# Optimization experiments

Hardware: AMD Instinct MI355X
Metric: run time of the kernel (lower is better)

## Reference

```python
import jax, jax.numpy as jnp
import numpy as np

D = 128
N_COLS = 64
EPS = 1e-6
# op MLP index per feature token: mult, add, cos, absdiff, sub_ab, sub_ba, div_ab, div_ba
MLP_IDX = np.array([0, 1, 2, 3, 4, 4, 5, 5])


def setup_inputs() -> dict:
    key = jax.random.key(0)
    ks = jax.random.split(key, 16)
    B = 64
    pairs = np.array([(i, j) for i in range(N_COLS) for j in range(i + 1, N_COLS)], dtype=np.int32)
    P = pairs.shape[0]  # 2016
    s = 0.02
    inp = {
        "x": jax.random.normal(ks[0], (B, N_COLS, D), dtype=jnp.float32),
        "presence": jax.random.randint(ks[1], (B, N_COLS), 0, 2, dtype=jnp.int32),
        "idx_i": jnp.asarray(pairs[:, 0]),
        "idx_j": jnp.asarray(pairs[:, 1]),
        # 6 op MLPs (multiply, add, cosine, abs_diff, subtract, divide): d -> d/2 -> d
        "ops_W1": jax.random.normal(ks[2], (6, D, D // 2), dtype=jnp.float32) * s,
        "ops_b1": jnp.zeros((6, D // 2), dtype=jnp.float32),
        "ops_W2": jax.random.normal(ks[3], (6, D // 2, D), dtype=jnp.float32) * s,
        "ops_b2": jnp.zeros((6, D), dtype=jnp.float32),
        # presence MLP: 4 -> d/2 -> d
        "pres_W1": jax.random.normal(ks[4], (4, D // 2), dtype=jnp.float32) * s,
        "pres_b1": jnp.zeros((D // 2,), dtype=jnp.float32),
        "pres_W2": jax.random.normal(ks[5], (D // 2, D), dtype=jnp.float32) * s,
        "pres_b2": jnp.zeros((D,), dtype=jnp.float32),
        # fusion MLP: 9d -> 2d -> d
        "fus_W1": jax.random.normal(ks[6], (9 * D, 2 * D), dtype=jnp.float32) * s,
        "fus_b1": jnp.zeros((2 * D,), dtype=jnp.float32),
        "fus_W2": jax.random.normal(ks[7], (2 * D, D), dtype=jnp.float32) * s,
        "fus_b2": jnp.zeros((D,), dtype=jnp.float32),
    }
    return inp


def reference(x, presence, idx_i, idx_j,
              ops_W1, ops_b1, ops_W2, ops_b2,
              pres_W1, pres_b1, pres_W2, pres_b2,
              fus_W1, fus_b1, fus_W2, fus_b2):
    B = x.shape[0]
    P = idx_i.shape[0]
    A = x[:, idx_i]  # [B, P, D]
    Bv = x[:, idx_j]  # [B, P, D]
    An = A / (jnp.linalg.norm(A, axis=-1, keepdims=True) + EPS)
    Bn = Bv / (jnp.linalg.norm(Bv, axis=-1, keepdims=True) + EPS)
    # 8 elementwise relation features [8, B, P, D]
    feats = jnp.stack([
        A * Bv,                 # multiply
        A + Bv,                 # add
        An * Bn,                # cosine (elementwise normalized product)
        jnp.abs(A - Bv),        # abs diff
        A - Bv,                 # subtract A->B
        Bv - A,                 # subtract B->A
        A / (Bv + EPS),         # divide A/B
        Bv / (A + EPS),         # divide B/A
    ])
    W1 = ops_W1[MLP_IDX]  # [8, D, D/2]
    b1 = ops_b1[MLP_IDX]
    W2 = ops_W2[MLP_IDX]
    b2 = ops_b2[MLP_IDX]
    h = jax.nn.relu(jnp.einsum('kbpd,kdh->kbph', feats, W1) + b1[:, None, None, :])
    tok = jnp.einsum('kbph,khd->kbpd', h, W2) + b2[:, None, None, :]  # [8, B, P, D]
    # presence flags [B, P, 4]
    pa = presence[:, idx_i].astype(x.dtype)
    pb = presence[:, idx_j].astype(x.dtype)
    flags = jnp.stack([pa * pb, pa * (1 - pb), (1 - pa) * pb, (1 - pa) * (1 - pb)], axis=-1)
    ptok = jax.nn.relu(flags @ pres_W1 + pres_b1) @ pres_W2 + pres_b2  # [B, P, D]
    # concat 9 tokens -> fusion MLP -> 1 token per pair
    cat = jnp.concatenate([jnp.transpose(tok, (1, 2, 0, 3)).reshape(B, P, 8 * D), ptok], axis=-1)
    out = jax.nn.relu(cat @ fus_W1 + fus_b1) @ fus_W2 + fus_b2  # [B, P, D]
    return out
```

## Files before the change

### kernel.cpp

```cpp
#include <hip/hip_runtime.h>

#define EPS 1e-6f

using bfrag = __attribute__((ext_vector_type(8))) short;
using ffrag = __attribute__((ext_vector_type(4))) float;
typedef unsigned short ushortT;

#define MFMA(a, b, c) __builtin_amdgcn_mfma_f32_16x16x32_bf16((a), (b), (c), 0, 0, 0)

__device__ __forceinline__ ushortT bf_hi(float x) {
  unsigned u = __builtin_bit_cast(unsigned, x);
  return (ushortT)((u + 0x7FFFu + ((u >> 16) & 1u)) >> 16);
}
__device__ __forceinline__ float uaf(unsigned u) { return __builtin_bit_cast(float, u); }
__device__ __forceinline__ unsigned cvtpk(float a, float b) {
  unsigned d;
  asm("v_cvt_pk_bf16_f32 %0, %1, %2" : "=v"(d) : "v"(a), "v"(b));
  return d;
}
__device__ __forceinline__ int op_of(int k) { return (k < 4) ? k : ((k >> 1) + 2); }

__global__ void prologue(const float* __restrict__ ops_W1,
                         const float* __restrict__ ops_W2,
                         const float* __restrict__ ops_b2,
                         const float* __restrict__ pres_W1,
                         const float* __restrict__ pres_b1,
                         const float* __restrict__ pres_W2,
                         const float* __restrict__ pres_b2,
                         const float* __restrict__ fus_W1,
                         const float* __restrict__ fus_b1,
                         const float* __restrict__ fus_W2,
                         ushortT* __restrict__ Gp,
                         ushortT* __restrict__ W1p,
                         ushortT* __restrict__ W2p,
                         float* __restrict__ cb) {
  const int blk = blockIdx.x;
  const int tid = threadIdx.x;

  if (blk < 512) {
    int r = blk, n = tid;
    int slot = r >> 6;
    const int KMAP[8] = {0, 2, 3, 4, 1, 5, 6, 7};
    int k = KMAP[slot];
    int op = op_of(k);
    const float* w2 = ops_W2 + (size_t)(op * 64 + (r & 63)) * 128;
    const float* w1 = fus_W1 + (size_t)(k * 128) * 256 + n;
    float a0 = 0.f, a1 = 0.f, a2 = 0.f, a3 = 0.f;
#pragma unroll 8
    for (int d = 0; d < 128; d += 4) {
      a0 = fmaf(w2[d], w1[(size_t)d * 256], a0);
      a1 = fmaf(w2[d + 1], w1[(size_t)(d + 1) * 256], a1);
      a2 = fmaf(w2[d + 2], w1[(size_t)(d + 2) * 256], a2);
      a3 = fmaf(w2[d + 3], w1[(size_t)(d + 3) * 256], a3);
    }
    float acc = (a0 + a1) + (a2 + a3);
    int nt = n >> 4, kk = r >> 5, quad = (r >> 3) & 3, j = r & 7;
    int lane = quad * 16 + (n & 15);
    Gp[((nt * 16 + kk) * 64 + lane) * 8 + j] = bf_hi(acc);
  } else if (blk < 544) {
    int gid = (blk - 512) * 256 + tid;
    int lane = gid & 63, kk = (gid >> 6) & 3, nt = (gid >> 8) & 3, k = gid >> 10;
    int op = op_of(k);
    int col = nt * 16 + (lane & 15);
#pragma unroll
    for (int j = 0; j < 8; ++j) {
      int d = kk * 32 + ((lane >> 4) & 3) * 8 + j;
      W1p[gid * 8 + j] = bf_hi(ops_W1[((size_t)op * 128 + d) * 64 + col]);
    }
  } else if (blk < 560) {
    int gid = (blk - 544) * 256 + tid;
    int lane = gid & 63, kk = (gid >> 6) & 7, nt = gid >> 9;
    int col = nt * 16 + (lane & 15);
#pragma unroll
    for (int j = 0; j < 8; ++j) {
      int d = kk * 32 + ((lane >> 4) & 3) * 8 + j;
      W2p[gid * 8 + j] = bf_hi(fus_W2[(size_t)d * 128 + col]);
    }
  } else {
    int c = blk - 560, n = tid;
    __shared__ float hrelu[64];
    __shared__ float ptok[128];
    if (n < 64) hrelu[n] = fmaxf(pres_W1[c * 64 + n] + pres_b1[n], 0.f);
    __syncthreads();
    if (n < 128) {
      float p0 = pres_b2[n], p1 = 0.f;
#pragma unroll 8
      for (int hh = 0; hh < 64; hh += 2) {
        p0 = fmaf(hrelu[hh], pres_W2[hh * 128 + n], p0);
        p1 = fmaf(hrelu[hh + 1], pres_W2[(hh + 1) * 128 + n], p1);
      }
      ptok[n] = p0 + p1;
    }
    __syncthreads();
    float acc = fus_b1[n];
#pragma unroll 4
    for (int d = 0; d < 128; ++d)
      acc = fmaf(ptok[d], fus_W1[(size_t)(1024 + d) * 256 + n], acc);
    float acc2 = 0.f;
    for (int k = 0; k < 8; ++k) {
      int op = op_of(k);
#pragma unroll 4
      for (int d = 0; d < 128; ++d)
        acc2 = fmaf(ops_b2[op * 128 + d], fus_W1[(size_t)(k * 128 + d) * 256 + n], acc2);
    }
    cb[c * 256 + n] = acc + acc2;
  }
}

__device__ __forceinline__ void ldX(const float* Xrow, int quad, float (&r)[32]) {
#pragma unroll
  for (int kk = 0; kk < 4; ++kk) {
    float4 t0 = *(const float4*)(Xrow + kk * 32 + quad * 8);
    float4 t1 = *(const float4*)(Xrow + kk * 32 + quad * 8 + 4);
    r[kk * 8 + 0] = t0.x; r[kk * 8 + 1] = t0.y; r[kk * 8 + 2] = t0.z; r[kk * 8 + 3] = t0.w;
    r[kk * 8 + 4] = t1.x; r[kk * 8 + 5] = t1.y; r[kk * 8 + 6] = t1.z; r[kk * 8 + 7] = t1.w;
  }
}

struct Frag2 {
  bfrag h[4];
  bfrag l[4];
};

union U4 {
  unsigned u[4];
  bfrag b;
};

#define FM_MUL 0
#define FM_ADD 1
#define FM_SUB 2
#define FM_ABS 3
#define FM_DAB 4
#define FM_DBA 5

template <int M>
__device__ __forceinline__ void buildFrags(const float (&af)[32], const float (&bf)[32],
                                           Frag2& fr) {
#pragma unroll
  for (int kk = 0; kk < 4; ++kk) {
    U4 uh, ul;
#pragma unroll
    for (int p = 0; p < 4; ++p) {
      float a0 = af[kk * 8 + 2 * p],     b0 = bf[kk * 8 + 2 * p];
      float a1 = af[kk * 8 + 2 * p + 1], b1 = bf[kk * 8 + 2 * p + 1];
      float f0, f1;
      if constexpr (M == FM_MUL)      { f0 = a0 * b0; f1 = a1 * b1; }
      else if constexpr (M == FM_ADD) { f0 = a0 + b0; f1 = a1 + b1; }
      else if constexpr (M == FM_SUB) { f0 = a0 - b0; f1 = a1 - b1; }
      else if constexpr (M == FM_ABS) { f0 = fabsf(a0 - b0); f1 = fabsf(a1 - b1); }
      else if constexpr (M == FM_DAB) {
        f0 = a0 * __builtin_amdgcn_rcpf(b0 + EPS);
        f1 = a1 * __builtin_amdgcn_rcpf(b1 + EPS);
      } else {
        f0 = b0 * __builtin_amdgcn_rcpf(a0 + EPS);
        f1 = b1 * __builtin_amdgcn_rcpf(a1 + EPS);
      }
      unsigned dh = cvtpk(f0, f1);
      float r0 = f0 - uaf(dh << 16);
      float r1 = f1 - uaf(dh & 0xFFFF0000u);
      uh.u[p] = dh;
      ul.u[p] = cvtpk(r0, r1);
    }
    fr.h[kk] = uh.b;
    fr.l[kk] = ul.b;
  }
}

template <int K>
__device__ __forceinline__ void mmAll(const Frag2& fr, int lane,
                                      const ushortT* __restrict__ W1p, ffrag (&s)[4]) {
#pragma unroll
  for (int nt = 0; nt < 4; ++nt) {
    const ushortT* wp = W1p + ((K * 4 + nt) * 4) * 512 + lane * 8;
    ffrag acc = {0.f, 0.f, 0.f, 0.f};
#pragma unroll
    for (int kk = 0; kk < 4; ++kk) {
      bfrag w = *(const bfrag*)(wp + kk * 512);
      acc = MFMA(fr.h[kk], w, acc);
      acc = MFMA(fr.l[kk], w, acc);
    }
    s[nt] = acc;
  }
}

__device__ __forceinline__ void ldBias(const float* __restrict__ ops_b1, int OP, int c0,
                                       float (&bb)[4]) {
#pragma unroll
  for (int nt = 0; nt < 4; ++nt) bb[nt] = ops_b1[OP * 64 + nt * 16 + c0];
}

__device__ __forceinline__ void storeH(ffrag s, float scl, float bias, int rbase, int col,
                                       ushortT (*Hh)[136], ushortT (*Hl)[136]) {
  float v[4];
#pragma unroll
  for (int i = 0; i < 4; ++i) v[i] = fmaxf(fmaf(s[i], scl, bias), 0.f);
#pragma unroll
  for (int p = 0; p < 2; ++p) {
    unsigned dh = cvtpk(v[2 * p], v[2 * p + 1]);
    float r0 = v[2 * p] - uaf(dh << 16);
    float r1 = v[2 * p + 1] - uaf(dh & 0xFFFF0000u);
    unsigned dl = cvtpk(r0, r1);
    Hh[rbase + 2 * p][col] = (ushortT)(dh & 0xFFFFu);
    Hh[rbase + 2 * p + 1][col] = (ushortT)(dh >> 16);
    Hl[rbase + 2 * p][col] = (ushortT)(dl & 0xFFFFu);
    Hl[rbase + 2 * p + 1][col] = (ushortT)(dl >> 16);
  }
}

__device__ __forceinline__ void storeH4(const ffrag (&s)[4], float scl, const float (&bb)[4],
                                        int rbase, int colbase, int c0,
                                        ushortT (*Hh)[136], ushortT (*Hl)[136]) {
#pragma unroll
  for (int nt = 0; nt < 4; ++nt)
    storeH(s[nt], scl, bb[nt], rbase, colbase + nt * 16 + c0, Hh, Hl);
}

__device__ __forceinline__ void p3round(int r, int wv, int lane, int quad, int c0,
                                        ushortT (*Hh)[136], ushortT (*Hl)[136],
                                        const ushortT* __restrict__ Gp,
                                        ffrag (&u)[4], ffrag (&v)[4]) {
#pragma unroll
  for (int kk = 0; kk < 4; ++kk) {
    bfrag ah0 = *(const bfrag*)&Hh[c0][kk * 32 + quad * 8];
    bfrag al0 = *(const bfrag*)&Hl[c0][kk * 32 + quad * 8];
    bfrag ah1 = *(const bfrag*)&Hh[16 + c0][kk * 32 + quad * 8];
    bfrag al1 = *(const bfrag*)&Hl[16 + c0][kk * 32 + quad * 8];
#pragma unroll
    for (int nt4 = 0; nt4 < 4; ++nt4) {
      bfrag g = *(const bfrag*)(Gp + (((wv * 4 + nt4) * 16 + r * 4 + kk) * 64 + lane) * 8);
      u[nt4] = MFMA(ah0, g, u[nt4]);
      u[nt4] = MFMA(al0, g, u[nt4]);
      v[nt4] = MFMA(ah1, g, v[nt4]);
      v[nt4] = MFMA(al1, g, v[nt4]);
    }
  }
}

__global__ __launch_bounds__(256, 3)
void drel_main(const float* __restrict__ x, const int* __restrict__ presence,
               const int* __restrict__ idx_i, const int* __restrict__ idx_j,
               const float* __restrict__ ops_b1, const float* __restrict__ fus_b2,
               const ushortT* __restrict__ W1p, const ushortT* __restrict__ Gp,
               const ushortT* __restrict__ W2p, const float* __restrict__ cbias,
               float* __restrict__ out) {
  __shared__ __align__(16) char smem[51328];
  float   (*Xs)[132]  = reinterpret_cast<float(*)[132]>(smem);
  ushortT (*Hh)[136]  = reinterpret_cast<ushortT(*)[136]>(smem + 33792);
  ushortT (*Hl)[136]  = reinterpret_cast<ushortT(*)[136]>(smem + 42496);
  ushortT (*Dh)[264]  = reinterpret_cast<ushortT(*)[264]>(smem + 33792);
  int* sCombo = reinterpret_cast<int*>(smem + 51200);

  const int tid = threadIdx.x;
  const int wv = tid >> 6, lane = tid & 63, quad = lane >> 4, c0 = lane & 15;
  const int wtile = wv & 1;
  const int wrole = wv >> 1;

  const int blk = blockIdx.x;
  const int b = blk / 63;
  const int p0 = (blk % 63) * 32;

  const float* xb = x + (size_t)b * 64 * 128;
#pragma unroll
  for (int it = 0; it < 8; ++it) {
    int i = tid + it * 256;
    int row = i >> 5, c4 = (i & 31) * 4;
    *(float4*)&Xs[row][c4] = *(const float4*)(xb + row * 128 + c4);
  }
  if (tid < 32) {
    int p = p0 + tid;
    int pa = presence[b * 64 + idx_i[p]];
    int pb = presence[b * 64 + idx_j[p]];
    sCombo[tid] = pa ? (pb ? 0 : 1) : (pb ? 2 : 3);
  }

  const int rI = idx_i[p0 + wtile * 16 + c0];
  const int rJ = idx_j[p0 + wtile * 16 + c0];
  const int rbase = wtile * 16 + quad * 4;

  ffrag u[4], v[4];
  __syncthreads();
  {
    int comb0[4], comb1[4];
#pragma unroll
    for (int i = 0; i < 4; ++i) {
      comb0[i] = sCombo[quad * 4 + i];
      comb1[i] = sCombo[16 + quad * 4 + i];
    }
#pragma unroll
    for (int nt4 = 0; nt4 < 4; ++nt4) {
      int col = (wv * 4 + nt4) * 16 + c0;
#pragma unroll
      for (int i = 0; i < 4; ++i) {
        u[nt4][i] = cbias[comb0[i] * 256 + col];
        v[nt4][i] = cbias[comb1[i] * 256 + col];
      }
    }
  }

  float af[32], bf[32];
  Frag2 fr;
  ffrag s4[4];

  {
    ldX(Xs[rI], quad, af); ldX(Xs[rJ], quad, bf);
    buildFrags<FM_MUL>(af, bf, fr);
    ffrag s[4];
    float bb[4];
    if (wrole == 0) {
      ldBias(ops_b1, 0, c0, bb);
      mmAll<0>(fr, lane, W1p, s);
      storeH4(s, 1.f, bb, rbase, 0, c0, Hh, Hl);
    } else {
      float sa = 0.f, sb = 0.f;
#pragma unroll
      for (int q = 0; q < 32; ++q) { sa = fmaf(af[q], af[q], sa); sb = fmaf(bf[q], bf[q], sb); }
      sa += __shfl_xor(sa, 16); sb += __shfl_xor(sb, 16);
      sa += __shfl_xor(sa, 32); sb += __shfl_xor(sb, 32);
      float scl = (1.f / (sqrtf(sa) + EPS)) * (1.f / (sqrtf(sb) + EPS));
      ldBias(ops_b1, 2, c0, bb);
      mmAll<2>(fr, lane, W1p, s);
      storeH4(s, scl, bb, rbase, 64, c0, Hh, Hl);
    }
  }
  __syncthreads();
  p3round(0, wv, lane, quad, c0, Hh, Hl, Gp, u, v);
  __syncthreads();

  {
    ldX(Xs[rI], quad, af); ldX(Xs[rJ], quad, bf);
    float bb[4];
    if (wrole == 0) {
      buildFrags<FM_ABS>(af, bf, fr);
      ffrag s[4];
      ldBias(ops_b1, 3, c0, bb);
      mmAll<3>(fr, lane, W1p, s);
      storeH4(s, 1.f, bb, rbase, 0, c0, Hh, Hl);
    } else {
      buildFrags<FM_SUB>(af, bf, fr);
      ldBias(ops_b1, 4, c0, bb);
      mmAll<4>(fr, lane, W1p, s4);
      storeH4(s4, 1.f, bb, rbase, 64, c0, Hh, Hl);
    }
  }
  __syncthreads();
  p3round(1, wv, lane, quad, c0, Hh, Hl, Gp, u, v);
  __syncthreads();

  {
    float bb[4];
    if (wrole == 0) {
      ldX(Xs[rI], quad, af); ldX(Xs[rJ], quad, bf);
      buildFrags<FM_ADD>(af, bf, fr);
      ffrag s[4];
      ldBias(ops_b1, 1, c0, bb);
      mmAll<1>(fr, lane, W1p, s);
      storeH4(s, 1.f, bb, rbase, 0, c0, Hh, Hl);
    } else {
      ldBias(ops_b1, 4, c0, bb);
      storeH4(s4, -1.f, bb, rbase, 64, c0, Hh, Hl);
    }
  }
  __syncthreads();
  p3round(2, wv, lane, quad, c0, Hh, Hl, Gp, u, v);
  __syncthreads();

  {
    ldX(Xs[rI], quad, af); ldX(Xs[rJ], quad, bf);
    ffrag s[4];
    float bb[4];
    ldBias(ops_b1, 5, c0, bb);
    if (wrole == 0) {
      buildFrags<FM_DAB>(af, bf, fr);
      mmAll<6>(fr, lane, W1p, s);
      storeH4(s, 1.f, bb, rbase, 0, c0, Hh, Hl);
    } else {
      buildFrags<FM_DBA>(af, bf, fr);
      mmAll<7>(fr, lane, W1p, s);
      storeH4(s, 1.f, bb, rbase, 64, c0, Hh, Hl);
    }
  }
  __syncthreads();
  p3round(3, wv, lane, quad, c0, Hh, Hl, Gp, u, v);
  __syncthreads();

#pragma unroll
  for (int nt4 = 0; nt4 < 4; ++nt4) {
    int col = (wv * 4 + nt4) * 16 + c0;
#pragma unroll
    for (int p = 0; p < 2; ++p) {
      unsigned du = cvtpk(fmaxf(u[nt4][2 * p], 0.f), fmaxf(u[nt4][2 * p + 1], 0.f));
      Dh[quad * 4 + 2 * p][col] = (ushortT)(du & 0xFFFFu);
      Dh[quad * 4 + 2 * p + 1][col] = (ushortT)(du >> 16);
      unsigned dv = cvtpk(fmaxf(v[nt4][2 * p], 0.f), fmaxf(v[nt4][2 * p + 1], 0.f));
      Dh[16 + quad * 4 + 2 * p][col] = (ushortT)(dv & 0xFFFFu);
      Dh[16 + quad * 4 + 2 * p + 1][col] = (ushortT)(dv >> 16);
    }
  }
  __syncthreads();

  ffrag o[2], q[2];
#pragma unroll
  for (int nt2 = 0; nt2 < 2; ++nt2) {
    float bias = fus_b2[(wv * 2 + nt2) * 16 + c0];
    o[nt2] = ffrag{bias, bias, bias, bias};
    q[nt2] = o[nt2];
  }
#pragma unroll
  for (int kk = 0; kk < 8; ++kk) {
    bfrag dh0 = *(const bfrag*)&Dh[c0][kk * 32 + quad * 8];
    bfrag dh1 = *(const bfrag*)&Dh[16 + c0][kk * 32 + quad * 8];
#pragma unroll
    for (int nt2 = 0; nt2 < 2; ++nt2) {
      bfrag w = *(const bfrag*)(W2p + (((wv * 2 + nt2) * 8 + kk) * 64 + lane) * 8);
      o[nt2] = MFMA(dh0, w, o[nt2]);
      q[nt2] = MFMA(dh1, w, q[nt2]);
    }
  }
#pragma unroll
  for (int nt2 = 0; nt2 < 2; ++nt2) {
    int col = (wv * 2 + nt2) * 16 + c0;
#pragma unroll
    for (int i = 0; i < 4; ++i) {
      int row = quad * 4 + i;
      out[(size_t)(b * 2016 + p0 + row) * 128 + col] = o[nt2][i];
      out[(size_t)(b * 2016 + p0 + 16 + row) * 128 + col] = q[nt2][i];
    }
  }
}

extern "C" void kernel_launch(void* const* d_in, const int* in_sizes, int n_in,
                              void* d_out, int out_size, void* d_ws, size_t ws_size,
                              hipStream_t stream) {
  const float* x        = (const float*)d_in[0];
  const int*   presence = (const int*)d_in[1];
  const int*   idx_i    = (const int*)d_in[2];
  const int*   idx_j    = (const int*)d_in[3];
  const float* ops_W1   = (const float*)d_in[4];
  const float* ops_b1   = (const float*)d_in[5];
  const float* ops_W2   = (const float*)d_in[6];
  const float* ops_b2   = (const float*)d_in[7];
  const float* pres_W1  = (const float*)d_in[8];
  const float* pres_b1  = (const float*)d_in[9];
  const float* pres_W2  = (const float*)d_in[10];
  const float* pres_b2  = (const float*)d_in[11];
  const float* fus_W1   = (const float*)d_in[12];
  const float* fus_b1   = (const float*)d_in[13];
  const float* fus_W2   = (const float*)d_in[14];
  const float* fus_b2   = (const float*)d_in[15];

  char* ws = (char*)d_ws;
  ushortT* Gp  = (ushortT*)(ws);
  ushortT* W1p = (ushortT*)(ws + 262144);
  ushortT* W2p = (ushortT*)(ws + 393216);
  float*   CB  = (float*)(ws + 458752);

  prologue<<<564, 256, 0, stream>>>(ops_W1, ops_W2, ops_b2, pres_W1, pres_b1,
                                    pres_W2, pres_b2, fus_W1, fus_b1, fus_W2,
                                    Gp, W1p, W2p, CB);
  drel_main<<<4032, 256, 0, stream>>>(x, presence, idx_i, idx_j, ops_b1, fus_b2,
                                      W1p, Gp, W2p, CB, (float*)d_out);
}
```

Measured before the change: 259.8 us.

## Use single-pass fp16 MFMA for bounded ops instead of split bf16 hi/lo

For the six well-bounded feature ops (mul, add, cos, abs, sub), the kernel now packs the features, the op W1 weights and the fused W2·fusW1 product into fp16 and does one fp16 MFMA per step. Before, it split each value into bf16 high and low parts and ran two bf16 MFMAs. The division ops keep the split-bf16 path because their values can be very large. This halves MFMA count and LDS traffic for most rounds. In exchange it takes on fp16 range and precision risk on the activations and weights.

```diff
diff --git a/kernel.cpp b/kernel.cpp
--- a/kernel.cpp
+++ b/kernel.cpp
@@ -3,10 +3,12 @@
 #define EPS 1e-6f
 
 using bfrag = __attribute__((ext_vector_type(8))) short;
+using hfrag = __attribute__((ext_vector_type(8))) _Float16;
 using ffrag = __attribute__((ext_vector_type(4))) float;
 typedef unsigned short ushortT;
 
 #define MFMA(a, b, c) __builtin_amdgcn_mfma_f32_16x16x32_bf16((a), (b), (c), 0, 0, 0)
+#define MFMA16(a, b, c) __builtin_amdgcn_mfma_f32_16x16x32_f16((a), (b), (c), 0, 0, 0)
 
 __device__ __forceinline__ ushortT bf_hi(float x) {
   unsigned u = __builtin_bit_cast(unsigned, x);
@@ -16,6 +18,11 @@
 __device__ __forceinline__ unsigned cvtpk(float a, float b) {
   unsigned d;
   asm("v_cvt_pk_bf16_f32 %0, %1, %2" : "=v"(d) : "v"(a), "v"(b));
+  return d;
+}
+__device__ __forceinline__ unsigned pkf16(float a, float b) {
+  unsigned d;
+  asm("v_cvt_pkrtz_f16_f32 %0, %1, %2" : "=v"(d) : "v"(a), "v"(b));
   return d;
 }
 __device__ __forceinline__ int op_of(int k) { return (k < 4) ? k : ((k >> 1) + 2); }
@@ -54,9 +61,16 @@
       a3 = fmaf(w2[d + 3], w1[(size_t)(d + 3) * 256], a3);
     }
     float acc = (a0 + a1) + (a2 + a3);
+    ushortT outv;
+    if (slot < 6) {
+      _Float16 hv = (_Float16)acc;
+      outv = __builtin_bit_cast(ushortT, hv);
+    } else {
+      outv = bf_hi(acc);
+    }
     int nt = n >> 4, kk = r >> 5, quad = (r >> 3) & 3, j = r & 7;
     int lane = quad * 16 + (n & 15);
-    Gp[((nt * 16 + kk) * 64 + lane) * 8 + j] = bf_hi(acc);
+    Gp[((nt * 16 + kk) * 64 + lane) * 8 + j] = outv;
   } else if (blk < 544) {
     int gid = (blk - 512) * 256 + tid;
     int lane = gid & 63, kk = (gid >> 6) & 3, nt = (gid >> 8) & 3, k = gid >> 10;
@@ -65,7 +79,15 @@
 #pragma unroll
     for (int j = 0; j < 8; ++j) {
       int d = kk * 32 + ((lane >> 4) & 3) * 8 + j;
-      W1p[gid * 8 + j] = bf_hi(ops_W1[((size_t)op * 128 + d) * 64 + col]);
+      float w = ops_W1[((size_t)op * 128 + d) * 64 + col];
+      ushortT outv;
+      if (k < 6) {
+        _Float16 hv = (_Float16)w;
+        outv = __builtin_bit_cast(ushortT, hv);
+      } else {
+        outv = bf_hi(w);
+      }
+      W1p[gid * 8 + j] = outv;
     }
   } else if (blk < 560) {
     int gid = (blk - 544) * 256 + tid;
@@ -135,11 +157,11 @@
 #define FM_DBA 5
 
 template <int M>
-__device__ __forceinline__ void buildFrags(const float (&af)[32], const float (&bf)[32],
-                                           Frag2& fr) {
+__device__ __forceinline__ void buildFragsF16(const float (&af)[32], const float (&bf)[32],
+                                              bfrag (&h)[4]) {
 #pragma unroll
   for (int kk = 0; kk < 4; ++kk) {
-    U4 uh, ul;
+    U4 uh;
 #pragma unroll
     for (int p = 0; p < 4; ++p) {
       float a0 = af[kk * 8 + 2 * p],     b0 = bf[kk * 8 + 2 * p];
@@ -148,8 +170,25 @@
       if constexpr (M == FM_MUL)      { f0 = a0 * b0; f1 = a1 * b1; }
       else if constexpr (M == FM_ADD) { f0 = a0 + b0; f1 = a1 + b1; }
       else if constexpr (M == FM_SUB) { f0 = a0 - b0; f1 = a1 - b1; }
-      else if constexpr (M == FM_ABS) { f0 = fabsf(a0 - b0); f1 = fabsf(a1 - b1); }
-      else if constexpr (M == FM_DAB) {
+      else                            { f0 = fabsf(a0 - b0); f1 = fabsf(a1 - b1); }
+      uh.u[p] = pkf16(f0, f1);
+    }
+    h[kk] = uh.b;
+  }
+}
+
+template <int M>
+__device__ __forceinline__ void buildFrags(const float (&af)[32], const float (&bf)[32],
+                                           Frag2& fr) {
+#pragma unroll
+  for (int kk = 0; kk < 4; ++kk) {
+    U4 uh, ul;
+#pragma unroll
+    for (int p = 0; p < 4; ++p) {
+      float a0 = af[kk * 8 + 2 * p],     b0 = bf[kk * 8 + 2 * p];
+      float a1 = af[kk * 8 + 2 * p + 1], b1 = bf[kk * 8 + 2 * p + 1];
+      float f0, f1;
+      if constexpr (M == FM_DAB) {
         f0 = a0 * __builtin_amdgcn_rcpf(b0 + EPS);
         f1 = a1 * __builtin_amdgcn_rcpf(b1 + EPS);
       } else {
@@ -168,6 +207,22 @@
 }
 
 template <int K>
+__device__ __forceinline__ void mmAllF16(const bfrag (&h)[4], int lane,
+                                         const ushortT* __restrict__ W1p, ffrag (&s)[4]) {
+#pragma unroll
+  for (int nt = 0; nt < 4; ++nt) {
+    const ushortT* wp = W1p + ((K * 4 + nt) * 4) * 512 + lane * 8;
+    ffrag acc = {0.f, 0.f, 0.f, 0.f};
+#pragma unroll
+    for (int kk = 0; kk < 4; ++kk) {
+      hfrag w = __builtin_bit_cast(hfrag, *(const bfrag*)(wp + kk * 512));
+      acc = MFMA16(__builtin_bit_cast(hfrag, h[kk]), w, acc);
+    }
+    s[nt] = acc;
+  }
+}
+
+template <int K>
 __device__ __forceinline__ void mmAll(const Frag2& fr, int lane,
                                       const ushortT* __restrict__ W1p, ffrag (&s)[4]) {
 #pragma unroll
@@ -190,11 +245,32 @@
   for (int nt = 0; nt < 4; ++nt) bb[nt] = ops_b1[OP * 64 + nt * 16 + c0];
 }
 
-__device__ __forceinline__ void storeH(ffrag s, float scl, float bias, int rbase, int col,
+__device__ __forceinline__ void storeHf(ffrag s, float scl, float bias, int rbase, int col,
+                                        ushortT (*Hh)[136]) {
+  float v[4];
+#pragma unroll
+  for (int i = 0; i < 4; ++i) v[i] = fmaxf(fmaf(s[i], scl, bias), 0.f);
+#pragma unroll
+  for (int p = 0; p < 2; ++p) {
+    unsigned d = pkf16(v[2 * p], v[2 * p + 1]);
+    Hh[rbase + 2 * p][col] = (ushortT)(d & 0xFFFFu);
+    Hh[rbase + 2 * p + 1][col] = (ushortT)(d >> 16);
+  }
+}
+
+__device__ __forceinline__ void storeHf4(const ffrag (&s)[4], float scl, const float (&bb)[4],
+                                         int rbase, int colbase, int c0,
+                                         ushortT (*Hh)[136]) {
+#pragma unroll
+  for (int nt = 0; nt < 4; ++nt)
+    storeHf(s[nt], scl, bb[nt], rbase, colbase + nt * 16 + c0, Hh);
+}
+
+__device__ __forceinline__ void storeH(ffrag s, float bias, int rbase, int col,
                                        ushortT (*Hh)[136], ushortT (*Hl)[136]) {
   float v[4];
 #pragma unroll
-  for (int i = 0; i < 4; ++i) v[i] = fmaxf(fmaf(s[i], scl, bias), 0.f);
+  for (int i = 0; i < 4; ++i) v[i] = fmaxf(s[i] + bias, 0.f);
 #pragma unroll
   for (int p = 0; p < 2; ++p) {
     unsigned dh = cvtpk(v[2 * p], v[2 * p + 1]);
@@ -208,12 +284,30 @@
   }
 }
 
-__device__ __forceinline__ void storeH4(const ffrag (&s)[4], float scl, const float (&bb)[4],
+__device__ __forceinline__ void storeH4(const ffrag (&s)[4], const float (&bb)[4],
                                         int rbase, int colbase, int c0,
                                         ushortT (*Hh)[136], ushortT (*Hl)[136]) {
 #pragma unroll
   for (int nt = 0; nt < 4; ++nt)
-    storeH(s[nt], scl, bb[nt], rbase, colbase + nt * 16 + c0, Hh, Hl);
+    storeH(s[nt], bb[nt], rbase, colbase + nt * 16 + c0, Hh, Hl);
+}
+
+__device__ __forceinline__ void p3roundF16(int r, int wv, int lane, int quad, int c0,
+                                           ushortT (*Hh)[136],
+                                           const ushortT* __restrict__ Gp,
+                                           ffrag (&u)[4], ffrag (&v)[4]) {
+#pragma unroll
+  for (int kk = 0; kk < 4; ++kk) {
+    hfrag ah0 = __builtin_bit_cast(hfrag, *(const bfrag*)&Hh[c0][kk * 32 + quad * 8]);
+    hfrag ah1 = __builtin_bit_cast(hfrag, *(const bfrag*)&Hh[16 + c0][kk * 32 + quad * 8]);
+#pragma unroll
+    for (int nt4 = 0; nt4 < 4; ++nt4) {
+      hfrag g = __builtin_bit_cast(
+          hfrag, *(const bfrag*)(Gp + (((wv * 4 + nt4) * 16 + r * 4 + kk) * 64 + lane) * 8));
+      u[nt4] = MFMA16(ah0, g, u[nt4]);
+      v[nt4] = MFMA16(ah1, g, v[nt4]);
+    }
+  }
 }
 
 __device__ __forceinline__ void p3round(int r, int wv, int lane, int quad, int c0,
@@ -299,18 +393,18 @@
   }
 
   float af[32], bf[32];
-  Frag2 fr;
+  bfrag fh[4];
   ffrag s4[4];
 
   {
     ldX(Xs[rI], quad, af); ldX(Xs[rJ], quad, bf);
-    buildFrags<FM_MUL>(af, bf, fr);
+    buildFragsF16<FM_MUL>(af, bf, fh);
     ffrag s[4];
     float bb[4];
     if (wrole == 0) {
       ldBias(ops_b1, 0, c0, bb);
-      mmAll<0>(fr, lane, W1p, s);
-      storeH4(s, 1.f, bb, rbase, 0, c0, Hh, Hl);
+      mmAllF16<0>(fh, lane, W1p, s);
+      storeHf4(s, 1.f, bb, rbase, 0, c0, Hh);
     } else {
       float sa = 0.f, sb = 0.f;
 #pragma unroll
@@ -319,65 +413,66 @@
       sa += __shfl_xor(sa, 32); sb += __shfl_xor(sb, 32);
       float scl = (1.f / (sqrtf(sa) + EPS)) * (1.f / (sqrtf(sb) + EPS));
       ldBias(ops_b1, 2, c0, bb);
-      mmAll<2>(fr, lane, W1p, s);
-      storeH4(s, scl, bb, rbase, 64, c0, Hh, Hl);
-    }
-  }
-  __syncthreads();
-  p3round(0, wv, lane, quad, c0, Hh, Hl, Gp, u, v);
+      mmAllF16<2>(fh, lane, W1p, s);
+      storeHf4(s, scl, bb, rbase, 64, c0, Hh);
+    }
+  }
+  __syncthreads();
+  p3roundF16(0, wv, lane, quad, c0, Hh, Gp, u, v);
   __syncthreads();
 
   {
     ldX(Xs[rI], quad, af); ldX(Xs[rJ], quad, bf);
     float bb[4];
     if (wrole == 0) {
-      buildFrags<FM_ABS>(af, bf, fr);
+      buildFragsF16<FM_ABS>(af, bf, fh);
       ffrag s[4];
       ldBias(ops_b1, 3, c0, bb);
-      mmAll<3>(fr, lane, W1p, s);
-      storeH4(s, 1.f, bb, rbase, 0, c0, Hh, Hl);
+      mmAllF16<3>(fh, lane, W1p, s);
+      storeHf4(s, 1.f, bb, rbase, 0, c0, Hh);
     } else {
-      buildFrags<FM_SUB>(af, bf, fr);
+      buildFragsF16<FM_SUB>(af, bf, fh);
       ldBias(ops_b1, 4, c0, bb);
-      mmAll<4>(fr, lane, W1p, s4);
-      storeH4(s4, 1.f, bb, rbase, 64, c0, Hh, Hl);
-    }
-  }
-  __syncthreads();
-  p3round(1, wv, lane, quad, c0, Hh, Hl, Gp, u, v);
+      mmAllF16<4>(fh, lane, W1p, s4);
+      storeHf4(s4, 1.f, bb, rbase, 64, c0, Hh);
+    }
+  }
+  __syncthreads();
+  p3roundF16(1, wv, lane, quad, c0, Hh, Gp, u, v);
   __syncthreads();
 
   {
     float bb[4];
     if (wrole == 0) {
       ldX(Xs[rI], quad, af); ldX(Xs[rJ], quad, bf);
-      buildFrags<FM_ADD>(af, bf, fr);
+      buildFragsF16<FM_ADD>(af, bf, fh);
       ffrag s[4];
       ldBias(ops_b1, 1, c0, bb);
-      mmAll<1>(fr, lane, W1p, s);
-      storeH4(s, 1.f, bb, rbase, 0, c0, Hh, Hl);
+      mmAllF16<1>(fh, lane, W1p, s);
+      storeHf4(s, 1.f, bb, rbase, 0, c0, Hh);
     } else {
       ldBias(ops_b1, 4, c0, bb);
-      storeH4(s4, -1.f, bb, rbase, 64, c0, Hh, Hl);
-    }
-  }
-  __syncthreads();
-  p3round(2, wv, lane, quad, c0, Hh, Hl, Gp, u, v);
+      storeHf4(s4, -1.f, bb, rbase, 64, c0, Hh);
+    }
+  }
+  __syncthreads();
+  p3roundF16(2, wv, lane, quad, c0, Hh, Gp, u, v);
   __syncthreads();
 
   {
     ldX(Xs[rI], quad, af); ldX(Xs[rJ], quad, bf);
+    Frag2 fr;
     ffrag s[4];
     float bb[4];
     ldBias(ops_b1, 5, c0, bb);
     if (wrole == 0) {
       buildFrags<FM_DAB>(af, bf, fr);
       mmAll<6>(fr, lane, W1p, s);
-      storeH4(s, 1.f, bb, rbase, 0, c0, Hh, Hl);
+      storeH4(s, bb, rbase, 0, c0, Hh, Hl);
     } else {
       buildFrags<FM_DBA>(af, bf, fr);
       mmAll<7>(fr, lane, W1p, s);
-      storeH4(s, 1.f, bb, rbase, 64, c0, Hh, Hl);
+      storeH4(s, bb, rbase, 64, c0, Hh, Hl);
     }
   }
   __syncthreads();
```

New measurement: 243.8 us. 1.07x faster.
